# Optimization experiments

Measured on AMD Instinct MI355X. Metric: run time of the kernel, lower is better.

## Reference

```python
import jax, jax.numpy as jnp
import numpy as np

N = 100000
E = 1600000
IN = 128
HEADS = 8
HID = 16  # out_channels // heads
NEG_SLOPE = 0.2


def setup_inputs() -> dict:
    key = jax.random.key(0)
    k1, k2, k3, k4, k5 = jax.random.split(key, 5)
    x = jax.random.normal(k1, (N, IN), dtype=jnp.float32)
    edge_index = jax.random.randint(k2, (2, E), 0, N, dtype=jnp.int32)
    pos = jax.random.uniform(k3, (N,), dtype=jnp.float32)  # positive per-node weights
    W = jax.random.normal(k4, (HEADS * HID, IN), dtype=jnp.float32) * 0.1  # lin.weight
    att = jax.random.normal(k5, (1, HEADS, 2 * HID), dtype=jnp.float32) * 0.1
    return {"x": x, "edge_index": edge_index, "pos": pos, "W": W, "att": att}


def reference(x, edge_index, pos, W, att):
    n = x.shape[0]
    hid = att.shape[-1] // 2
    heads = att.shape[1]
    # linear projection: [N, heads, hid]
    h = (x @ W.T).reshape(n, heads, hid)
    row, col = edge_index[0], edge_index[1]
    # cat([h[row], h[col]], -1) * att -> sum(-1) == h[row].att_l + h[col].att_r
    att_l = att[0, :, :hid]   # [heads, hid]
    att_r = att[0, :, hid:]   # [heads, hid]
    al = jnp.einsum('nhd,hd->nh', h, att_l)  # [N, heads]
    ar = jnp.einsum('nhd,hd->nh', h, att_r)
    alpha = al[row] + ar[col]                # [E, heads]
    alpha = jnp.where(alpha >= 0, alpha, NEG_SLOPE * alpha)  # LeakyReLU
    # softmax_weights: exp, scale by pos[col], normalize by scatter row-sum
    alpha = jnp.exp(alpha) * pos[col][:, None]
    rowsum = jax.ops.segment_sum(alpha, row, num_segments=n)  # [N, heads]
    inv = 1.0 / rowsum + 1e-16
    alpha = alpha * inv[row]
    # weighted scatter-add aggregation
    out = jax.ops.segment_sum(alpha[:, :, None] * h[col], row, num_segments=n)
    return out.reshape(n, heads * hid)  # concat=True
```

## Files before the change

### kernel.cpp

```cpp
#include <hip/hip_runtime.h>
#include <hip/hip_fp16.h>


#define BK    512
#define BSH   9
#define NBMAX 256
#define BCAP  9216
#define EPB   16

typedef _Float16 half8 __attribute__((ext_vector_type(8)));
typedef float    f32x4 __attribute__((ext_vector_type(4)));

__global__ __launch_bounds__(256) void prep_w(
        const float* __restrict__ W, _Float16* __restrict__ WBh,
        _Float16* __restrict__ WBl) {
    int i = blockIdx.x * 256 + threadIdx.x;
    if (i < 16384) {
        const int j    = i & 7;
        const int lane = (i >> 3) & 63;
        const int ct   = (i >> 9) & 7;
        const int ks   = i >> 12;
        const int nn   = lane & 15;
        const int kg   = lane >> 4;
        const float w  = W[(ct * 16 + nn) * 128 + ks * 32 + kg * 8 + j];
        const _Float16 hi = (_Float16)w;
        WBh[i] = hi;
        WBl[i] = (_Float16)(w - (float)hi);
    }
}

__global__ __launch_bounds__(256) void node_h(
        const float* __restrict__ x, const _Float16* __restrict__ WBh,
        const _Float16* __restrict__ WBl, const float* __restrict__ att,
        const float* __restrict__ pos,
        _Float16* __restrict__ h, float* __restrict__ al,
        float* __restrict__ arp, int n) {
    const int t    = threadIdx.x;
    const int wv   = t >> 6;
    const int lane = t & 63;
    const int m    = lane & 15;
    const int kg   = lane >> 4;
    const int nodeA = blockIdx.x * 64 + wv * 16 + m;
    const bool avalid = nodeA < n;

    f32x4 acc[8];
#pragma unroll
    for (int ct = 0; ct < 8; ++ct) acc[ct] = (f32x4)0.f;

    const half8* bh = (const half8*)WBh;
    const half8* bl = (const half8*)WBl;

#pragma unroll
    for (int ks = 0; ks < 4; ++ks) {
        float xv[8];
        if (avalid) {
            const float4* xp =
                (const float4*)&x[(size_t)nodeA * 128 + ks * 32 + kg * 8];
            *(float4*)&xv[0] = xp[0];
            *(float4*)&xv[4] = xp[1];
        } else {
#pragma unroll
            for (int j = 0; j < 8; ++j) xv[j] = 0.f;
        }
        half8 axh, axl;
#pragma unroll
        for (int j = 0; j < 8; ++j) {
            const _Float16 hi = (_Float16)xv[j];
            axh[j] = hi;
            axl[j] = (_Float16)(xv[j] - (float)hi);
        }
#pragma unroll
        for (int ct = 0; ct < 8; ++ct) {
            const half8 bhv = bh[(ks * 8 + ct) * 64 + lane];
            const half8 blv = bl[(ks * 8 + ct) * 64 + lane];
            acc[ct] = __builtin_amdgcn_mfma_f32_16x16x32_f16(axl, bhv, acc[ct], 0, 0, 0);
            acc[ct] = __builtin_amdgcn_mfma_f32_16x16x32_f16(axh, blv, acc[ct], 0, 0, 0);
            acc[ct] = __builtin_amdgcn_mfma_f32_16x16x32_f16(axh, bhv, acc[ct], 0, 0, 0);
        }
    }

    const int nodeD0 = blockIdx.x * 64 + wv * 16 + kg * 4;
#pragma unroll
    for (int r = 0; r < 4; ++r) {
        const int node = nodeD0 + r;
        if (node < n) {
#pragma unroll
            for (int ct = 0; ct < 8; ++ct)
                h[(size_t)node * 128 + ct * 16 + m] = (_Float16)acc[ct][r];
        }
    }

    float attl[8], attr[8];
#pragma unroll
    for (int ct = 0; ct < 8; ++ct) {
        attl[ct] = att[ct * 32 + m];
        attr[ct] = att[ct * 32 + 16 + m];
    }
#pragma unroll
    for (int r = 0; r < 4; ++r) {
        const int node = nodeD0 + r;
#pragma unroll
        for (int ct = 0; ct < 8; ++ct) {
            float pl = acc[ct][r] * attl[ct];
            float pr = acc[ct][r] * attr[ct];
            pl += __shfl_xor(pl, 1, 64); pl += __shfl_xor(pl, 2, 64);
            pl += __shfl_xor(pl, 4, 64); pl += __shfl_xor(pl, 8, 64);
            pr += __shfl_xor(pr, 1, 64); pr += __shfl_xor(pr, 2, 64);
            pr += __shfl_xor(pr, 4, 64); pr += __shfl_xor(pr, 8, 64);
            if (m == 0 && node < n) {
                al[node * 8 + ct] = pl;
                arp[(size_t)node * 16 + ct] = pr;
            }
        }
        if (m == 0 && node < n)
            arp[(size_t)node * 16 + 8] = pos[node];
    }
}

__global__ __launch_bounds__(256) void bin_edges(
        const int* __restrict__ ei, int* __restrict__ gcur,
        int* __restrict__ bins, int E, int nb) {
    __shared__ int  cnt[NBMAX];
    __shared__ int  basep[NBMAX];
    __shared__ int  lstart[NBMAX];
    __shared__ int2 sorted[256 * EPB];
    const int t    = threadIdx.x;
    const int base = blockIdx.x * (256 * EPB);
    cnt[t] = 0;
    __syncthreads();

    int rr[EPB], off[EPB];
#pragma unroll
    for (int j = 0; j < EPB; ++j) {
        const int e = base + j * 256 + t;
        if (e < E) {
            rr[j]  = ei[e];
            off[j] = atomicAdd(&cnt[rr[j] >> BSH], 1);
        } else rr[j] = -1;
    }
    __syncthreads();
    const int v = cnt[t];
    lstart[t] = v;
    __syncthreads();
    for (int o = 1; o < 256; o <<= 1) {
        const int tmp = (t >= o) ? lstart[t - o] : 0;
        __syncthreads();
        lstart[t] += tmp;
        __syncthreads();
    }
    const int incl = lstart[t];
    __syncthreads();
    lstart[t] = incl - v;
    basep[t]  = (t < nb && v > 0) ? atomicAdd(&gcur[t], v) : 0;
    __syncthreads();

#pragma unroll
    for (int j = 0; j < EPB; ++j) {
        if (rr[j] >= 0) {
            const int e = base + j * 256 + t;
            const int b = rr[j] >> BSH;
            sorted[lstart[b] + off[j]] = make_int2(ei[E + e], rr[j]);
        }
    }
    __syncthreads();

    const int total = lstart[255] + cnt[255];
    for (int i = t; i < total; i += 256) {
        const int2 p = sorted[i];
        const int  b = p.y >> BSH;
        const int  q = basep[b] + i - lstart[b];
        if (q < BCAP)
            bins[(size_t)b * BCAP + q] = p.x | ((p.y & (BK - 1)) << 17);
    }
}

__global__ __launch_bounds__(256) void scan_top(
        const int* __restrict__ gcur, int* __restrict__ bbase, int nb) {
    __shared__ int s[256];
    const int t = threadIdx.x;
    const int v = (t < nb) ? min(gcur[t], BCAP) : 0;
    s[t] = v;
    __syncthreads();
    for (int o = 1; o < 256; o <<= 1) {
        const int tmp = (t >= o) ? s[t - o] : 0;
        __syncthreads();
        s[t] += tmp;
        __syncthreads();
    }
    if (t < nb) bbase[t] = s[t] - v;
}

__global__ __launch_bounds__(512) void bucket_fill(
        const int* __restrict__ bins, const int* __restrict__ gcur,
        const int* __restrict__ bbase, int* __restrict__ rowstart,
        int* __restrict__ rowend, int* __restrict__ csr, int n) {
    __shared__ int ld[BK], sc[BK], cur[BK];
    const int b = blockIdx.x, t = threadIdx.x;
    ld[t] = 0;
    __syncthreads();
    const int cnt = min(gcur[b], BCAP);
    const int* bp = bins + (size_t)b * BCAP;
    for (int i = t; i < cnt; i += 512)
        atomicAdd(&ld[((unsigned)bp[i]) >> 17], 1);
    __syncthreads();
    const int v = ld[t];
    sc[t] = v;
    __syncthreads();
    for (int o = 1; o < 512; o <<= 1) {
        const int tmp = (t >= o) ? sc[t - o] : 0;
        __syncthreads();
        sc[t] += tmp;
        __syncthreads();
    }
    const int node = b * BK + t;
    const int s0   = sc[t] - v + bbase[b];
    cur[t] = s0;
    if (node < n) rowstart[node] = s0;
    __syncthreads();
    for (int i = t; i < cnt; i += 512) {
        const int vv = bp[i];
        const int q  = atomicAdd(&cur[((unsigned)vv) >> 17], 1);
        csr[q] = vv & 0x1FFFF;
    }
    __syncthreads();
    if (node < n) rowend[node] = cur[t];
}

__global__ __launch_bounds__(256) void row_gather(
        const int* __restrict__ csr, const int* __restrict__ rowstart,
        const int* __restrict__ rowend,
        const float* __restrict__ al, const float* __restrict__ arp,
        const _Float16* __restrict__ h, float* __restrict__ out, int n) {
    const int r    = (blockIdx.x * 256 + threadIdx.x) >> 6;
    const int lane = threadIdx.x & 63;
    if (r >= n) return;
    const int s = rowstart[r];
    const int e = rowend[r];
    const int sl = lane & 15;
    if (s >= e) {
        if (lane < 16) {
            float4 z = make_float4(0.f, 0.f, 0.f, 0.f);
            *(float4*)&out[(size_t)r * 128 + sl * 8]     = z;
            *(float4*)&out[(size_t)r * 128 + sl * 8 + 4] = z;
        }
        return;
    }
    const int   head = sl >> 1;
    const float al_l = (sl < 8) ? al[r * 8 + sl] : 0.f;
    float acc[8];
#pragma unroll
    for (int i = 0; i < 8; ++i) acc[i] = 0.f;
    float rs = 0.f;
#pragma unroll 2
    for (int j = s; j < e; j += 4) {
        const int  jj    = j + (lane >> 4);
        const bool valid = jj < e;
        const int  c     = csr[valid ? jj : s];
        float av = 0.f;
        if (sl < 8 && valid) {
            const float* ap = &arp[(size_t)c * 16];
            float a = al_l + ap[sl];
            a  = (a >= 0.f) ? a : 0.2f * a;
            av = __expf(a) * ap[8];
            rs += av;
        }
        const float alpha = __shfl(av, (lane & 48) + head, 64);
        float4 hv = *(const float4*)&h[(size_t)c * 128 + sl * 8];
        const __half2* hp = (const __half2*)&hv;
        const float2 f0 = __half22float2(hp[0]);
        const float2 f1 = __half22float2(hp[1]);
        const float2 f2 = __half22float2(hp[2]);
        const float2 f3 = __half22float2(hp[3]);
        acc[0] = fmaf(alpha, f0.x, acc[0]);
        acc[1] = fmaf(alpha, f0.y, acc[1]);
        acc[2] = fmaf(alpha, f1.x, acc[2]);
        acc[3] = fmaf(alpha, f1.y, acc[3]);
        acc[4] = fmaf(alpha, f2.x, acc[4]);
        acc[5] = fmaf(alpha, f2.y, acc[5]);
        acc[6] = fmaf(alpha, f3.x, acc[6]);
        acc[7] = fmaf(alpha, f3.y, acc[7]);
    }
    rs += __shfl_xor(rs, 16, 64);
    rs += __shfl_xor(rs, 32, 64);
#pragma unroll
    for (int i = 0; i < 8; ++i) {
        acc[i] += __shfl_xor(acc[i], 16, 64);
        acc[i] += __shfl_xor(acc[i], 32, 64);
    }
    const float rsh = __shfl(rs, (lane & 48) + head, 64);
    const float sc  = (rsh != 0.f) ? (1.f / rsh + 1e-16f) : 0.f;
    if (lane < 16) {
        float4 o0 = make_float4(acc[0] * sc, acc[1] * sc, acc[2] * sc, acc[3] * sc);
        float4 o1 = make_float4(acc[4] * sc, acc[5] * sc, acc[6] * sc, acc[7] * sc);
        *(float4*)&out[(size_t)r * 128 + sl * 8]     = o0;
        *(float4*)&out[(size_t)r * 128 + sl * 8 + 4] = o1;
    }
}

extern "C" void kernel_launch(void* const* d_in, const int* in_sizes, int n_in,
                              void* d_out, int out_size, void* d_ws, size_t ws_size,
                              hipStream_t stream) {
    const float* x   = nullptr;
    const int*   ei  = nullptr;
    const float* pos = nullptr;
    const float* W   = nullptr;
    const float* att = nullptr;
    int E2 = 0;
    for (int i = 0; i < n_in; ++i) {
        int s = in_sizes[i];
        if      (s == out_size)        x   = (const float*)d_in[i];
        else if (s == out_size / 128)  pos = (const float*)d_in[i];
        else if (s == 16384)           W   = (const float*)d_in[i];
        else if (s == 256)             att = (const float*)d_in[i];
        else { ei = (const int*)d_in[i]; E2 = s; }
    }
    float* out = (float*)d_out;
    const int N_ = out_size / 128;
    const int E_ = E2 / 2;
    const int NB = (N_ + BK - 1) / BK;

    _Float16* h   = (_Float16*)d_ws;
    float* al     = (float*)(h + (size_t)N_ * 128);
    float* arp    = al + (size_t)N_ * 8;
    _Float16* WBh = (_Float16*)(arp + (size_t)N_ * 16);
    _Float16* WBl = WBh + 16384;
    int* rowstart = (int*)(WBl + 16384);
    int* rowend   = rowstart + N_;
    int* bbase    = rowend + N_;
    int* gcur     = bbase + NBMAX;
    int* csr      = gcur + NBMAX;
    int* bins     = csr + E_;

    hipMemsetAsync(gcur, 0, (size_t)NBMAX * sizeof(int), stream);

    prep_w<<<64, 256, 0, stream>>>(W, WBh, WBl);
    node_h<<<(N_ + 63) / 64, 256, 0, stream>>>(x, WBh, WBl, att, pos,
                                               h, al, arp, N_);
    bin_edges<<<(E_ + 256 * EPB - 1) / (256 * EPB), 256, 0, stream>>>(
        ei, gcur, bins, E_, NB);
    scan_top<<<1, 256, 0, stream>>>(gcur, bbase, NB);
    bucket_fill<<<NB, 512, 0, stream>>>(bins, gcur, bbase, rowstart, rowend,
                                        csr, N_);
    row_gather<<<(N_ * 64 + 255) / 256, 256, 0, stream>>>(
        csr, rowstart, rowend, al, arp, h, out, N_);
}
```

Before: 283.2 us.

## Fold attention projections into GEMM, shrink buckets, drop scan kernel, compact arp

Precomputes W·att as a ninth MFMA column tile so node_h produces al/ar directly, replacing the shuffle reductions. The ar values are stored as fp16 in a compact 8-half array and pos is read separately in row_gather, which shrinks the per-edge gather footprint. Buckets are halved to 256 nodes with 512 of them and bin_edges now runs 512-thread blocks. The separate scan_top kernel is removed; each bucket_fill block computes its own base by reducing the preceding counts. Storing ar in fp16 adds precision risk, and the redundant per-block prefix sums add some work.

```diff
diff --git a/kernel.cpp b/kernel.cpp
--- a/kernel.cpp
+++ b/kernel.cpp
@@ -2,39 +2,49 @@
 #include <hip/hip_fp16.h>
 
 
-#define BK    512
-#define BSH   9
-#define NBMAX 256
-#define BCAP  9216
-#define EPB   16
+#define BK    256
+#define BSH   8
+#define NBMAX 512
+#define BCAP  4736
+#define EPB   8
 
 typedef _Float16 half8 __attribute__((ext_vector_type(8)));
 typedef float    f32x4 __attribute__((ext_vector_type(4)));
 
 __global__ __launch_bounds__(256) void prep_w(
-        const float* __restrict__ W, _Float16* __restrict__ WBh,
-        _Float16* __restrict__ WBl) {
+        const float* __restrict__ W, const float* __restrict__ att,
+        _Float16* __restrict__ WBh, _Float16* __restrict__ WBl) {
     int i = blockIdx.x * 256 + threadIdx.x;
-    if (i < 16384) {
-        const int j    = i & 7;
-        const int lane = (i >> 3) & 63;
-        const int ct   = (i >> 9) & 7;
-        const int ks   = i >> 12;
-        const int nn   = lane & 15;
-        const int kg   = lane >> 4;
-        const float w  = W[(ct * 16 + nn) * 128 + ks * 32 + kg * 8 + j];
-        const _Float16 hi = (_Float16)w;
-        WBh[i] = hi;
-        WBl[i] = (_Float16)(w - (float)hi);
-    }
+    if (i >= 4 * 9 * 64 * 8) return;
+    const int j    = i & 7;
+    const int lane = (i >> 3) & 63;
+    const int ctks = i >> 9;
+    const int ct   = ctks % 9;
+    const int ks   = ctks / 9;
+    const int nn   = lane & 15;
+    const int kg   = lane >> 4;
+    const int k    = ks * 32 + kg * 8 + j;
+    float w;
+    if (ct < 8) {
+        w = W[(ct * 16 + nn) * 128 + k];
+    } else {
+        const int head = nn & 7;
+        const int sel  = nn >> 3;
+        float s = 0.f;
+        for (int d = 0; d < 16; ++d)
+            s += att[head * 32 + sel * 16 + d] * W[(head * 16 + d) * 128 + k];
+        w = s;
+    }
+    const _Float16 hi = (_Float16)w;
+    WBh[i] = hi;
+    WBl[i] = (_Float16)(w - (float)hi);
 }
 
 __global__ __launch_bounds__(256) void node_h(
         const float* __restrict__ x, const _Float16* __restrict__ WBh,
-        const _Float16* __restrict__ WBl, const float* __restrict__ att,
-        const float* __restrict__ pos,
+        const _Float16* __restrict__ WBl,
         _Float16* __restrict__ h, float* __restrict__ al,
-        float* __restrict__ arp, int n) {
+        _Float16* __restrict__ arh, int n) {
     const int t    = threadIdx.x;
     const int wv   = t >> 6;
     const int lane = t & 63;
@@ -43,9 +53,9 @@
     const int nodeA = blockIdx.x * 64 + wv * 16 + m;
     const bool avalid = nodeA < n;
 
-    f32x4 acc[8];
-#pragma unroll
-    for (int ct = 0; ct < 8; ++ct) acc[ct] = (f32x4)0.f;
+    f32x4 acc[9];
+#pragma unroll
+    for (int ct = 0; ct < 9; ++ct) acc[ct] = (f32x4)0.f;
 
     const half8* bh = (const half8*)WBh;
     const half8* bl = (const half8*)WBl;
@@ -70,9 +80,9 @@
             axl[j] = (_Float16)(xv[j] - (float)hi);
         }
 #pragma unroll
-        for (int ct = 0; ct < 8; ++ct) {
-            const half8 bhv = bh[(ks * 8 + ct) * 64 + lane];
-            const half8 blv = bl[(ks * 8 + ct) * 64 + lane];
+        for (int ct = 0; ct < 9; ++ct) {
+            const half8 bhv = bh[(ks * 9 + ct) * 64 + lane];
+            const half8 blv = bl[(ks * 9 + ct) * 64 + lane];
             acc[ct] = __builtin_amdgcn_mfma_f32_16x16x32_f16(axl, bhv, acc[ct], 0, 0, 0);
             acc[ct] = __builtin_amdgcn_mfma_f32_16x16x32_f16(axh, blv, acc[ct], 0, 0, 0);
             acc[ct] = __builtin_amdgcn_mfma_f32_16x16x32_f16(axh, bhv, acc[ct], 0, 0, 0);
@@ -87,52 +97,28 @@
 #pragma unroll
             for (int ct = 0; ct < 8; ++ct)
                 h[(size_t)node * 128 + ct * 16 + m] = (_Float16)acc[ct][r];
-        }
-    }
-
-    float attl[8], attr[8];
-#pragma unroll
-    for (int ct = 0; ct < 8; ++ct) {
-        attl[ct] = att[ct * 32 + m];
-        attr[ct] = att[ct * 32 + 16 + m];
-    }
-#pragma unroll
-    for (int r = 0; r < 4; ++r) {
-        const int node = nodeD0 + r;
-#pragma unroll
-        for (int ct = 0; ct < 8; ++ct) {
-            float pl = acc[ct][r] * attl[ct];
-            float pr = acc[ct][r] * attr[ct];
-            pl += __shfl_xor(pl, 1, 64); pl += __shfl_xor(pl, 2, 64);
-            pl += __shfl_xor(pl, 4, 64); pl += __shfl_xor(pl, 8, 64);
-            pr += __shfl_xor(pr, 1, 64); pr += __shfl_xor(pr, 2, 64);
-            pr += __shfl_xor(pr, 4, 64); pr += __shfl_xor(pr, 8, 64);
-            if (m == 0 && node < n) {
-                al[node * 8 + ct] = pl;
-                arp[(size_t)node * 16 + ct] = pr;
-            }
-        }
-        if (m == 0 && node < n)
-            arp[(size_t)node * 16 + 8] = pos[node];
-    }
-}
-
-__global__ __launch_bounds__(256) void bin_edges(
+            if (m < 8) al[node * 8 + m] = acc[8][r];
+            else       arh[node * 8 + (m - 8)] = (_Float16)acc[8][r];
+        }
+    }
+}
+
+__global__ __launch_bounds__(512) void bin_edges(
         const int* __restrict__ ei, int* __restrict__ gcur,
         int* __restrict__ bins, int E, int nb) {
     __shared__ int  cnt[NBMAX];
     __shared__ int  basep[NBMAX];
     __shared__ int  lstart[NBMAX];
-    __shared__ int2 sorted[256 * EPB];
+    __shared__ int2 sorted[512 * EPB];
     const int t    = threadIdx.x;
-    const int base = blockIdx.x * (256 * EPB);
+    const int base = blockIdx.x * (512 * EPB);
     cnt[t] = 0;
     __syncthreads();
 
     int rr[EPB], off[EPB];
 #pragma unroll
     for (int j = 0; j < EPB; ++j) {
-        const int e = base + j * 256 + t;
+        const int e = base + j * 512 + t;
         if (e < E) {
             rr[j]  = ei[e];
             off[j] = atomicAdd(&cnt[rr[j] >> BSH], 1);
@@ -142,7 +128,7 @@
     const int v = cnt[t];
     lstart[t] = v;
     __syncthreads();
-    for (int o = 1; o < 256; o <<= 1) {
+    for (int o = 1; o < 512; o <<= 1) {
         const int tmp = (t >= o) ? lstart[t - o] : 0;
         __syncthreads();
         lstart[t] += tmp;
@@ -157,15 +143,15 @@
 #pragma unroll
     for (int j = 0; j < EPB; ++j) {
         if (rr[j] >= 0) {
-            const int e = base + j * 256 + t;
+            const int e = base + j * 512 + t;
             const int b = rr[j] >> BSH;
             sorted[lstart[b] + off[j]] = make_int2(ei[E + e], rr[j]);
         }
     }
     __syncthreads();
 
-    const int total = lstart[255] + cnt[255];
-    for (int i = t; i < total; i += 256) {
+    const int total = lstart[511] + cnt[511];
+    for (int i = t; i < total; i += 512) {
         const int2 p = sorted[i];
         const int  b = p.y >> BSH;
         const int  q = basep[b] + i - lstart[b];
@@ -174,50 +160,44 @@
     }
 }
 
-__global__ __launch_bounds__(256) void scan_top(
-        const int* __restrict__ gcur, int* __restrict__ bbase, int nb) {
-    __shared__ int s[256];
-    const int t = threadIdx.x;
-    const int v = (t < nb) ? min(gcur[t], BCAP) : 0;
-    s[t] = v;
-    __syncthreads();
-    for (int o = 1; o < 256; o <<= 1) {
-        const int tmp = (t >= o) ? s[t - o] : 0;
-        __syncthreads();
-        s[t] += tmp;
-        __syncthreads();
-    }
-    if (t < nb) bbase[t] = s[t] - v;
-}
-
-__global__ __launch_bounds__(512) void bucket_fill(
+__global__ __launch_bounds__(256) void bucket_fill(
         const int* __restrict__ bins, const int* __restrict__ gcur,
-        const int* __restrict__ bbase, int* __restrict__ rowstart,
-        int* __restrict__ rowend, int* __restrict__ csr, int n) {
+        int* __restrict__ rowstart, int* __restrict__ rowend,
+        int* __restrict__ csr, int n, int nb) {
     __shared__ int ld[BK], sc[BK], cur[BK];
     const int b = blockIdx.x, t = threadIdx.x;
+    int pv = 0;
+    for (int i = t; i < b; i += 256) pv += min(gcur[i], BCAP);
+    sc[t] = pv;
+    __syncthreads();
+    for (int o = 128; o > 0; o >>= 1) {
+        if (t < o) sc[t] += sc[t + o];
+        __syncthreads();
+    }
+    const int bbase = sc[0];
+    __syncthreads();
     ld[t] = 0;
     __syncthreads();
     const int cnt = min(gcur[b], BCAP);
     const int* bp = bins + (size_t)b * BCAP;
-    for (int i = t; i < cnt; i += 512)
+    for (int i = t; i < cnt; i += 256)
         atomicAdd(&ld[((unsigned)bp[i]) >> 17], 1);
     __syncthreads();
     const int v = ld[t];
     sc[t] = v;
     __syncthreads();
-    for (int o = 1; o < 512; o <<= 1) {
+    for (int o = 1; o < 256; o <<= 1) {
         const int tmp = (t >= o) ? sc[t - o] : 0;
         __syncthreads();
         sc[t] += tmp;
         __syncthreads();
     }
     const int node = b * BK + t;
-    const int s0   = sc[t] - v + bbase[b];
+    const int s0   = sc[t] - v + bbase;
     cur[t] = s0;
     if (node < n) rowstart[node] = s0;
     __syncthreads();
-    for (int i = t; i < cnt; i += 512) {
+    for (int i = t; i < cnt; i += 256) {
         const int vv = bp[i];
         const int q  = atomicAdd(&cur[((unsigned)vv) >> 17], 1);
         csr[q] = vv & 0x1FFFF;
@@ -229,8 +209,9 @@
 __global__ __launch_bounds__(256) void row_gather(
         const int* __restrict__ csr, const int* __restrict__ rowstart,
         const int* __restrict__ rowend,
-        const float* __restrict__ al, const float* __restrict__ arp,
-        const _Float16* __restrict__ h, float* __restrict__ out, int n) {
+        const float* __restrict__ al, const _Float16* __restrict__ arh,
+        const float* __restrict__ pos, const _Float16* __restrict__ h,
+        float* __restrict__ out, int n) {
     const int r    = (blockIdx.x * 256 + threadIdx.x) >> 6;
     const int lane = threadIdx.x & 63;
     if (r >= n) return;
@@ -258,10 +239,9 @@
         const int  c     = csr[valid ? jj : s];
         float av = 0.f;
         if (sl < 8 && valid) {
-            const float* ap = &arp[(size_t)c * 16];
-            float a = al_l + ap[sl];
+            float a = al_l + (float)arh[(size_t)c * 8 + sl];
             a  = (a >= 0.f) ? a : 0.2f * a;
-            av = __expf(a) * ap[8];
+            av = __expf(a) * pos[c];
             rs += av;
         }
         const float alpha = __shfl(av, (lane & 48) + head, 64);
@@ -320,27 +300,24 @@
     const int NB = (N_ + BK - 1) / BK;
 
     _Float16* h   = (_Float16*)d_ws;
-    float* al     = (float*)(h + (size_t)N_ * 128);
-    float* arp    = al + (size_t)N_ * 8;
-    _Float16* WBh = (_Float16*)(arp + (size_t)N_ * 16);
-    _Float16* WBl = WBh + 16384;
-    int* rowstart = (int*)(WBl + 16384);
+    float*    al  = (float*)(h + (size_t)N_ * 128);
+    _Float16* arh = (_Float16*)(al + (size_t)N_ * 8);
+    _Float16* WBh = arh + (size_t)N_ * 8;
+    _Float16* WBl = WBh + 18432;
+    int* rowstart = (int*)(WBl + 18432);
     int* rowend   = rowstart + N_;
-    int* bbase    = rowend + N_;
-    int* gcur     = bbase + NBMAX;
+    int* gcur     = rowend + N_;
     int* csr      = gcur + NBMAX;
     int* bins     = csr + E_;
 
     hipMemsetAsync(gcur, 0, (size_t)NBMAX * sizeof(int), stream);
 
-    prep_w<<<64, 256, 0, stream>>>(W, WBh, WBl);
-    node_h<<<(N_ + 63) / 64, 256, 0, stream>>>(x, WBh, WBl, att, pos,
-                                               h, al, arp, N_);
-    bin_edges<<<(E_ + 256 * EPB - 1) / (256 * EPB), 256, 0, stream>>>(
+    prep_w<<<72, 256, 0, stream>>>(W, att, WBh, WBl);
+    node_h<<<(N_ + 63) / 64, 256, 0, stream>>>(x, WBh, WBl, h, al, arh, N_);
+    bin_edges<<<(E_ + 512 * EPB - 1) / (512 * EPB), 512, 0, stream>>>(
         ei, gcur, bins, E_, NB);
-    scan_top<<<1, 256, 0, stream>>>(gcur, bbase, NB);
-    bucket_fill<<<NB, 512, 0, stream>>>(bins, gcur, bbase, rowstart, rowend,
-                                        csr, N_);
+    bucket_fill<<<NB, 256, 0, stream>>>(bins, gcur, rowstart, rowend,
+                                        csr, N_, NB);
     row_gather<<<(N_ * 64 + 255) / 256, 256, 0, stream>>>(
-        csr, rowstart, rowend, al, arp, h, out, N_);
-}
+        csr, rowstart, rowend, al, arh, pos, h, out, N_);
+}
```

Result: faster. 259.9 us (-8.2%).
